# Performance work log

Measured on AMD Instinct MI355X. Metric: run time of the kernel, lower is better.

## Reference

```python
import jax, jax.numpy as jnp
import numpy as np

INPUTS = 6
GROUPS = 10
EPS = 1e-4

def setup_inputs() -> dict:
    key = jax.random.key(0)
    k1, k2, k3 = jax.random.split(key, 3)
    B = 1048576
    out = jax.random.normal(k1, (B, GROUPS * INPUTS), dtype=jnp.float32)
    # 10 Linear(6,1) layers stacked: W [10,6], b [10]
    bound = 1.0 / np.sqrt(INPUTS)
    W = jax.random.uniform(k2, (GROUPS, INPUTS), jnp.float32, -bound, bound)
    b = jax.random.uniform(k3, (GROUPS,), jnp.float32, -bound, bound)
    gamma = jnp.ones((GROUPS,), jnp.float32)
    beta = jnp.zeros((GROUPS,), jnp.float32)
    return {"out": out, "W": W, "b": b, "gamma": gamma, "beta": beta}

def reference(out, W, b, gamma, beta):
    B = out.shape[0]
    # grouped matmul: [B,10,6] x [10,6] -> [B,10]
    x = out[:, : GROUPS * INPUTS].reshape(B, GROUPS, INPUTS)
    y = jnp.einsum('bgi,gi->bg', x, W) + b  # [B,10]
    # BatchNorm1d training mode: batch mean, biased variance, eps=1e-4
    mean = jnp.mean(y, axis=0)
    var = jnp.mean((y - mean) ** 2, axis=0)
    y_hat = (y - mean) * jax.lax.rsqrt(var + EPS)
    return y_hat * gamma + beta
```

## Files before the change

kernel.cpp:

```cpp
#include <hip/hip_runtime.h>
#include <math.h>

#define GROUPS 10
#define INPUTS 6
#define COLS (GROUPS * INPUTS)
#define EPSV 1e-4f

#define TNT 64
#define TROWS 64
#define TF4 (TROWS * 15)
#define TPB 8

#define NT2 1024

#define K3T 128
#define K3PL 5

#define NB1 2048
#define NT 256

typedef float nfloat4 __attribute__((ext_vector_type(4)));

__device__ inline unsigned bf16pair(float a, float b) {
    unsigned ua = __float_as_uint(a);
    unsigned ub = __float_as_uint(b);
    ua += 0x7fffu + ((ua >> 16) & 1u);
    ub += 0x7fffu + ((ub >> 16) & 1u);
    return (ua >> 16) | (ub & 0xffff0000u);
}

__global__ __launch_bounds__(TNT) void k1_staged(
    const float* __restrict__ in,
    const float* __restrict__ Wp,
    const float* __restrict__ bp,
    unsigned* __restrict__ y16,
    float* __restrict__ partials,
    int ntiles)
{
    __shared__ float4 tile[TF4];
    __shared__ uint4  ybuf4[TROWS * 5 / 4];
    unsigned* ybuf = reinterpret_cast<unsigned*>(ybuf4);
    const int tid = threadIdx.x;

    float Wr[COLS];
#pragma unroll
    for (int j = 0; j < COLS; ++j) Wr[j] = Wp[j];
    float br[GROUPS];
#pragma unroll
    for (int g = 0; g < GROUPS; ++g) br[g] = bp[g];

    float s[GROUPS], sq[GROUPS];
#pragma unroll
    for (int g = 0; g < GROUPS; ++g) { s[g] = 0.f; sq[g] = 0.f; }

    const int t0 = blockIdx.x * TPB;
    const int t1 = (t0 + TPB < ntiles) ? (t0 + TPB) : ntiles;

    for (int t = t0; t < t1; ++t) {
        const float4* src = reinterpret_cast<const float4*>(in) + (size_t)t * TF4;

        __syncthreads();
#pragma unroll
        for (int j = 0; j < 15; ++j)
            tile[j * TNT + tid] = src[j * TNT + tid];
        __syncthreads();

        const float* x = reinterpret_cast<const float*>(&tile[tid * 15]);
        float y[GROUPS];
#pragma unroll
        for (int g = 0; g < GROUPS; ++g) {
            float acc = br[g];
#pragma unroll
            for (int i = 0; i < INPUTS; ++i)
                acc = fmaf(x[g * INPUTS + i], Wr[g * INPUTS + i], acc);
            y[g] = acc;
            s[g] += acc;
            sq[g] = fmaf(acc, acc, sq[g]);
        }

#pragma unroll
        for (int j = 0; j < 5; ++j)
            ybuf[tid * 5 + j] = bf16pair(y[2 * j], y[2 * j + 1]);
        uint4 w      = ybuf4[tid];
        unsigned wt  = ybuf[256 + tid];

        unsigned* dst = y16 + (size_t)t * (TROWS * 5);
        reinterpret_cast<uint4*>(dst)[tid] = w;
        dst[256 + tid] = wt;
    }

#pragma unroll
    for (int off = 32; off > 0; off >>= 1) {
#pragma unroll
        for (int g = 0; g < GROUPS; ++g) {
            s[g]  += __shfl_down(s[g],  off, 64);
            sq[g] += __shfl_down(sq[g], off, 64);
        }
    }
    if (tid == 0) {
        float* p = partials + (size_t)blockIdx.x * (2 * GROUPS);
#pragma unroll
        for (int g = 0; g < GROUPS; ++g) {
            p[g]          = s[g];
            p[GROUPS + g] = sq[g];
        }
    }
}

__global__ __launch_bounds__(NT2) void k2_finalize(
    const float* __restrict__ partials, int nblocks,
    const float* __restrict__ gamma, const float* __restrict__ beta,
    float* __restrict__ ss, float invB)
{
    const int tid = threadIdx.x;
    float acc[2 * GROUPS];
#pragma unroll
    for (int j = 0; j < 2 * GROUPS; ++j) acc[j] = 0.f;

    for (int blk = tid; blk < nblocks; blk += NT2) {
        const float* p = partials + (size_t)blk * (2 * GROUPS);
#pragma unroll
        for (int j = 0; j < 2 * GROUPS; ++j) acc[j] += p[j];
    }

#pragma unroll
    for (int off = 32; off > 0; off >>= 1) {
#pragma unroll
        for (int j = 0; j < 2 * GROUPS; ++j)
            acc[j] += __shfl_down(acc[j], off, 64);
    }

    __shared__ float ls[NT2 / 64][2 * GROUPS];
    const int lane = tid & 63;
    const int wid  = tid >> 6;
    if (lane == 0) {
#pragma unroll
        for (int j = 0; j < 2 * GROUPS; ++j) ls[wid][j] = acc[j];
    }
    __syncthreads();
    if (tid < GROUPS) {
        float sum = 0.f, sumq = 0.f;
#pragma unroll
        for (int w = 0; w < NT2 / 64; ++w) {
            sum  += ls[w][tid];
            sumq += ls[w][GROUPS + tid];
        }
        float mean = sum * invB;
        float var  = sumq * invB - mean * mean;
        float sc   = gamma[tid] * rsqrtf(var + EPSV);
        ss[tid]          = sc;
        ss[GROUPS + tid] = beta[tid] - mean * sc;
    }
}

__global__ __launch_bounds__(K3T) void k3_normalize_bf16(
    const uint4* __restrict__ y8,
    const float* __restrict__ ss,
    float* __restrict__ outf,
    int n8)
{
    __shared__ float sc[GROUPS], sh[GROUPS];
    if (threadIdx.x < GROUPS) {
        sc[threadIdx.x] = ss[threadIdx.x];
        sh[threadIdx.x] = ss[GROUPS + threadIdx.x];
    }
    __syncthreads();

    nfloat4* out4 = reinterpret_cast<nfloat4*>(outf);

    const int base = blockIdx.x * (K3T * K3PL) + threadIdx.x;
#pragma unroll
    for (int k = 0; k < K3PL; ++k) {
        const int q = base + k * K3T;
        if (q < n8) {
            uint4 v = y8[q];
            float e[8];
            e[0] = __uint_as_float(v.x << 16);
            e[1] = __uint_as_float(v.x & 0xffff0000u);
            e[2] = __uint_as_float(v.y << 16);
            e[3] = __uint_as_float(v.y & 0xffff0000u);
            e[4] = __uint_as_float(v.z << 16);
            e[5] = __uint_as_float(v.z & 0xffff0000u);
            e[6] = __uint_as_float(v.w << 16);
            e[7] = __uint_as_float(v.w & 0xffff0000u);

            const int e0 = (q * 8) % GROUPS;
            float r[8];
#pragma unroll
            for (int j = 0; j < 8; ++j) {
                int g = e0 + j;
                if (g >= GROUPS) g -= GROUPS;
                r[j] = fmaf(e[j], sc[g], sh[g]);
            }
            nfloat4 lo = { r[0], r[1], r[2], r[3] };
            nfloat4 hi = { r[4], r[5], r[6], r[7] };
            __builtin_nontemporal_store(lo, &out4[2 * q]);
            __builtin_nontemporal_store(hi, &out4[2 * q + 1]);
        }
    }
}

__global__ __launch_bounds__(NT) void k1_compute(
    const float* __restrict__ in, const float* __restrict__ Wp,
    const float* __restrict__ bp, float* __restrict__ y_out,
    float* __restrict__ partials, int B)
{
    const int tid = threadIdx.x;
    const int gid = blockIdx.x * NT + tid;
    const int stride = gridDim.x * NT;

    float Wr[COLS];
#pragma unroll
    for (int j = 0; j < COLS; ++j) Wr[j] = Wp[j];
    float br[GROUPS];
#pragma unroll
    for (int g = 0; g < GROUPS; ++g) br[g] = bp[g];

    float s[GROUPS], sq[GROUPS];
#pragma unroll
    for (int g = 0; g < GROUPS; ++g) { s[g] = 0.f; sq[g] = 0.f; }

    for (int r = gid; r < B; r += stride) {
        const float4* row4 = reinterpret_cast<const float4*>(in + (size_t)r * COLS);
        float4 v[15];
#pragma unroll
        for (int j = 0; j < 15; ++j) v[j] = row4[j];
        const float* x = reinterpret_cast<const float*>(v);
        float y[GROUPS];
#pragma unroll
        for (int g = 0; g < GROUPS; ++g) {
            float acc = br[g];
#pragma unroll
            for (int i = 0; i < INPUTS; ++i)
                acc = fmaf(x[g * INPUTS + i], Wr[g * INPUTS + i], acc);
            y[g] = acc;
            s[g] += acc;
            sq[g] = fmaf(acc, acc, sq[g]);
        }
        float2* yo = reinterpret_cast<float2*>(y_out + (size_t)r * GROUPS);
#pragma unroll
        for (int j = 0; j < 5; ++j) yo[j] = make_float2(y[2 * j], y[2 * j + 1]);
    }

#pragma unroll
    for (int off = 32; off > 0; off >>= 1) {
#pragma unroll
        for (int g = 0; g < GROUPS; ++g) {
            s[g]  += __shfl_down(s[g],  off, 64);
            sq[g] += __shfl_down(sq[g], off, 64);
        }
    }
    __shared__ float ls[NT / 64][2 * GROUPS];
    const int lane = tid & 63;
    const int wid  = tid >> 6;
    if (lane == 0) {
#pragma unroll
        for (int g = 0; g < GROUPS; ++g) {
            ls[wid][g]          = s[g];
            ls[wid][GROUPS + g] = sq[g];
        }
    }
    __syncthreads();
    if (tid < 2 * GROUPS) {
        float t = ls[0][tid] + ls[1][tid] + ls[2][tid] + ls[3][tid];
        partials[(size_t)blockIdx.x * (2 * GROUPS) + tid] = t;
    }
}

__global__ __launch_bounds__(NT) void k3_normalize(
    const float4* __restrict__ y4, const float* __restrict__ ss,
    float4* __restrict__ out4, int n4)
{
    __shared__ float sc[GROUPS], sh[GROUPS];
    if (threadIdx.x < GROUPS) {
        sc[threadIdx.x] = ss[threadIdx.x];
        sh[threadIdx.x] = ss[GROUPS + threadIdx.x];
    }
    __syncthreads();
    int gid = blockIdx.x * NT + threadIdx.x;
    int stride = gridDim.x * NT;
    for (int q = gid; q < n4; q += stride) {
        float4 v = y4[q];
        int g0 = (q * 4) % GROUPS;
        int g1 = g0 + 1; if (g1 >= GROUPS) g1 -= GROUPS;
        int g2 = g1 + 1; if (g2 >= GROUPS) g2 -= GROUPS;
        int g3 = g2 + 1; if (g3 >= GROUPS) g3 -= GROUPS;
        v.x = fmaf(v.x, sc[g0], sh[g0]);
        v.y = fmaf(v.y, sc[g1], sh[g1]);
        v.z = fmaf(v.z, sc[g2], sh[g2]);
        v.w = fmaf(v.w, sc[g3], sh[g3]);
        out4[q] = v;
    }
}

extern "C" void kernel_launch(void* const* d_in, const int* in_sizes, int n_in,
                              void* d_out, int out_size, void* d_ws, size_t ws_size,
                              hipStream_t stream)
{
    const float* in    = (const float*)d_in[0];
    const float* W     = (const float*)d_in[1];
    const float* bias  = (const float*)d_in[2];
    const float* gamma = (const float*)d_in[3];
    const float* beta  = (const float*)d_in[4];
    float* out = (float*)d_out;

    const int B = in_sizes[0] / COLS;
    char* ws = (char*)d_ws;

    if ((B % (TROWS * TPB)) == 0) {
        const int ntiles = B / TROWS;
        const int nb1    = ntiles / TPB;

        const size_t yBytes    = (size_t)B * GROUPS * 2;
        const size_t partBytes = (size_t)nb1 * 2 * GROUPS * sizeof(float);
        size_t off = 0;
        unsigned* y16   = (unsigned*)(ws + off); off += yBytes;
        off = (off + 255) & ~(size_t)255;
        float* partials = (float*)(ws + off);    off += partBytes;
        float* ss       = (float*)(ws + off);    off += 2 * GROUPS * sizeof(float);

        if (ws_size >= off) {
            k1_staged<<<nb1, TNT, 0, stream>>>(in, W, bias, y16, partials, ntiles);
            k2_finalize<<<1, NT2, 0, stream>>>(partials, nb1, gamma, beta, ss,
                                               1.0f / (float)B);
            const int n8  = (B * GROUPS) / 8;
            const int nb3 = (n8 + K3T * K3PL - 1) / (K3T * K3PL);
            k3_normalize_bf16<<<nb3, K3T, 0, stream>>>(
                (const uint4*)y16, ss, out, n8);
            return;
        }
    }

    {
        float* fws = (float*)d_ws;
        const size_t yFloats    = (size_t)B * GROUPS;
        const size_t partFloats = (size_t)NB1 * 2 * GROUPS;
        float* y_ws     = fws;
        float* partials = fws + yFloats;
        float* ss       = partials + partFloats;
        k1_compute<<<NB1, NT, 0, stream>>>(in, W, bias, y_ws, partials, B);
        k2_finalize<<<1, NT2, 0, stream>>>(partials, NB1, gamma, beta, ss, 1.0f / (float)B);
        const int n4 = (B * GROUPS) / 4;
        k3_normalize<<<2048, NT, 0, stream>>>((const float4*)y_ws, ss, (float4*)out, n4);
    }
}
```

Baseline: 70.32 us.

## Double-buffer input tiles with global_load_lds DMA and drop nontemporal stores

Adds a k1 variant that loads each 64-row input tile straight from global memory into LDS with the global_load_lds builtin, double-buffered so the next tile's load overlaps compute on the current one, synchronised with manual vmcnt waits. It is meant to remove the register round-trip and the __syncthreads stalls of the staged load. The normalize kernel also switches from nontemporal stores to plain float4 stores. The hand-tuned vmcnt counts assume a fixed instruction count and can race if the compiler emits a different number of vector memory ops. There is also no workgroup barrier between the LDS loads and the reads of the tile, which looks unsafe.

```diff
diff --git a/kernel.cpp b/kernel.cpp
--- a/kernel.cpp
+++ b/kernel.cpp
@@ -19,7 +19,14 @@
 #define NB1 2048
 #define NT 256
 
-typedef float nfloat4 __attribute__((ext_vector_type(4)));
+#if defined(__has_builtin)
+#if __has_builtin(__builtin_amdgcn_global_load_lds)
+#define HAVE_GLL 1
+#endif
+#endif
+#ifndef HAVE_GLL
+#define HAVE_GLL 0
+#endif
 
 __device__ inline unsigned bf16pair(float a, float b) {
     unsigned ua = __float_as_uint(a);
@@ -28,6 +35,109 @@
     ub += 0x7fffu + ((ub >> 16) & 1u);
     return (ua >> 16) | (ub & 0xffff0000u);
 }
+
+#if HAVE_GLL
+__device__ inline void gll16(const float4* g, float4* l) {
+    __builtin_amdgcn_global_load_lds(
+        (__attribute__((address_space(1))) void*)(g),
+        (__attribute__((address_space(3))) void*)(l),
+        16, 0, 0);
+}
+
+__global__ __launch_bounds__(TNT) void k1_dma(
+    const float* __restrict__ in,
+    const float* __restrict__ Wp,
+    const float* __restrict__ bp,
+    unsigned* __restrict__ y16,
+    float* __restrict__ partials,
+    int ntiles)
+{
+    __shared__ float4 tileA[TF4];
+    __shared__ float4 tileB[TF4];
+    __shared__ uint4  ybuf4[TROWS * 5 / 4];
+    unsigned* ybuf = reinterpret_cast<unsigned*>(ybuf4);
+    const int tid = threadIdx.x;
+    const float4* in4 = reinterpret_cast<const float4*>(in);
+
+    float Wr[COLS];
+#pragma unroll
+    for (int j = 0; j < COLS; ++j) Wr[j] = Wp[j];
+    float br[GROUPS];
+#pragma unroll
+    for (int g = 0; g < GROUPS; ++g) br[g] = bp[g];
+
+    float s[GROUPS], sq[GROUPS];
+#pragma unroll
+    for (int g = 0; g < GROUPS; ++g) { s[g] = 0.f; sq[g] = 0.f; }
+
+    const int t0 = blockIdx.x * TPB;
+
+    {
+        const float4* src = in4 + (size_t)t0 * TF4;
+#pragma unroll
+        for (int j = 0; j < 15; ++j)
+            gll16(src + j * TNT + tid, &tileA[j * TNT]);
+    }
+
+#pragma unroll
+    for (int t = 0; t < TPB; ++t) {
+        float4* cur = (t & 1) ? tileB : tileA;
+        float4* nxt = (t & 1) ? tileA : tileB;
+
+        if (t + 1 < TPB) {
+            const float4* src = in4 + (size_t)(t0 + t + 1) * TF4;
+#pragma unroll
+            for (int j = 0; j < 15; ++j)
+                gll16(src + j * TNT + tid, &nxt[j * TNT]);
+        }
+
+        if (t == 0)            asm volatile("s_waitcnt vmcnt(15)" ::: "memory");
+        else if (t < TPB - 1)  asm volatile("s_waitcnt vmcnt(17)" ::: "memory");
+        else                   asm volatile("s_waitcnt vmcnt(2)"  ::: "memory");
+        __builtin_amdgcn_sched_barrier(0);
+
+        const float* x = reinterpret_cast<const float*>(&cur[tid * 15]);
+        float y[GROUPS];
+#pragma unroll
+        for (int g = 0; g < GROUPS; ++g) {
+            float acc = br[g];
+#pragma unroll
+            for (int i = 0; i < INPUTS; ++i)
+                acc = fmaf(x[g * INPUTS + i], Wr[g * INPUTS + i], acc);
+            y[g] = acc;
+            s[g] += acc;
+            sq[g] = fmaf(acc, acc, sq[g]);
+        }
+
+#pragma unroll
+        for (int j = 0; j < 5; ++j)
+            ybuf[tid * 5 + j] = bf16pair(y[2 * j], y[2 * j + 1]);
+        uint4 w      = ybuf4[tid];
+        unsigned wt  = ybuf[256 + tid];
+
+        unsigned* dst = y16 + (size_t)(t0 + t) * (TROWS * 5);
+        reinterpret_cast<uint4*>(dst)[tid] = w;
+        dst[256 + tid] = wt;
+    }
+
+#pragma unroll
+    for (int off = 32; off > 0; off >>= 1) {
+#pragma unroll
+        for (int g = 0; g < GROUPS; ++g) {
+            s[g]  += __shfl_down(s[g],  off, 64);
+            sq[g] += __shfl_down(sq[g], off, 64);
+        }
+    }
+    if (tid == 0) {
+        float* p = partials + (size_t)blockIdx.x * (2 * GROUPS);
+#pragma unroll
+        for (int g = 0; g < GROUPS; ++g) {
+            p[g]          = s[g];
+            p[GROUPS + g] = sq[g];
+        }
+    }
+}
+#endif
 
 __global__ __launch_bounds__(TNT) void k1_staged(
     const float* __restrict__ in,
@@ -58,7 +168,6 @@
 
     for (int t = t0; t < t1; ++t) {
         const float4* src = reinterpret_cast<const float4*>(in) + (size_t)t * TF4;
-
         __syncthreads();
 #pragma unroll
         for (int j = 0; j < 15; ++j)
@@ -83,7 +192,6 @@
             ybuf[tid * 5 + j] = bf16pair(y[2 * j], y[2 * j + 1]);
         uint4 w      = ybuf4[tid];
         unsigned wt  = ybuf[256 + tid];
-
         unsigned* dst = y16 + (size_t)t * (TROWS * 5);
         reinterpret_cast<uint4*>(dst)[tid] = w;
         dst[256 + tid] = wt;
@@ -156,7 +264,7 @@
 __global__ __launch_bounds__(K3T) void k3_normalize_bf16(
     const uint4* __restrict__ y8,
     const float* __restrict__ ss,
-    float* __restrict__ outf,
+    float4* __restrict__ out4,
     int n8)
 {
     __shared__ float sc[GROUPS], sh[GROUPS];
@@ -165,8 +273,6 @@
         sh[threadIdx.x] = ss[GROUPS + threadIdx.x];
     }
     __syncthreads();
-
-    nfloat4* out4 = reinterpret_cast<nfloat4*>(outf);
 
     const int base = blockIdx.x * (K3T * K3PL) + threadIdx.x;
 #pragma unroll
@@ -192,10 +298,8 @@
                 if (g >= GROUPS) g -= GROUPS;
                 r[j] = fmaf(e[j], sc[g], sh[g]);
             }
-            nfloat4 lo = { r[0], r[1], r[2], r[3] };
-            nfloat4 hi = { r[4], r[5], r[6], r[7] };
-            __builtin_nontemporal_store(lo, &out4[2 * q]);
-            __builtin_nontemporal_store(hi, &out4[2 * q + 1]);
+            out4[2 * q]     = make_float4(r[0], r[1], r[2], r[3]);
+            out4[2 * q + 1] = make_float4(r[4], r[5], r[6], r[7]);
         }
     }
 }
@@ -320,13 +424,17 @@
         float* ss       = (float*)(ws + off);    off += 2 * GROUPS * sizeof(float);
 
         if (ws_size >= off) {
+#if HAVE_GLL
+            k1_dma<<<nb1, TNT, 0, stream>>>(in, W, bias, y16, partials, ntiles);
+#else
             k1_staged<<<nb1, TNT, 0, stream>>>(in, W, bias, y16, partials, ntiles);
+#endif
             k2_finalize<<<1, NT2, 0, stream>>>(partials, nb1, gamma, beta, ss,
                                                1.0f / (float)B);
             const int n8  = (B * GROUPS) / 8;
             const int nb3 = (n8 + K3T * K3PL - 1) / (K3T * K3PL);
             k3_normalize_bf16<<<nb3, K3T, 0, stream>>>(
-                (const uint4*)y16, ss, out, n8);
+                (const uint4*)y16, ss, (float4*)out, n8);
             return;
         }
     }
```

New measurement: 72.58 us. 1.03x slower.
